# Optimization experiments

Hardware: AMD Instinct MI355X
Metric: run time of the kernel (lower is better)

## Reference

```python
import jax, jax.numpy as jnp
import numpy as np

FLTRSTDEV = 2.0
EXTGRADFAC = 10.0
DMAX = 15.0
ENHANCEMENT = 2.0   # enhancement_factor in the module
NEG_WEIGHT = 1.5    # negative_weight in the module


def make_gauss_edge_fltr(stdev: float) -> np.ndarray:
    """Gaussian-derivative edge filter, shape [2, 1, k, k] (OIHW), k = 2*ceil(2*stdev)+1."""
    r = int(np.ceil(2.0 * stdev))
    x = np.arange(-r, r + 1, dtype=np.float32)
    g = np.exp(-x ** 2 / (2.0 * stdev ** 2)).astype(np.float32)
    g /= g.sum()
    dg = (-x / (stdev ** 2)) * np.exp(-x ** 2 / (2.0 * stdev ** 2))
    dg = (dg / np.abs(dg).sum()).astype(np.float32)
    f_dy = np.outer(dg, g)   # gradient along axis 0
    f_dx = np.outer(g, dg)   # gradient along axis 1
    return np.stack([f_dy, f_dx])[:, None]  # [2,1,k,k]


def cmpt_grad_im(img, fltr):
    """img: [B,1,H,W], fltr: [2,1,k,k] -> [B,2,H,W] gradient image (SAME conv)."""
    return jax.lax.conv_general_dilated(
        img, fltr, window_strides=(1, 1), padding='SAME',
        dimension_numbers=('NCHW', 'OIHW', 'NCHW'))


def setup_inputs() -> dict:
    key = jax.random.key(0)
    k1, k2 = jax.random.split(key)
    B, H, W = 16, 1024, 1024
    # predicted signed distance map, roughly in [-DMAX, DMAX]
    pred_dmap = jax.random.normal(k1, (B, 1, H, W), dtype=jnp.float32) * 5.0
    # stand-in for the snake-rendered signed distance map (detached target)
    snake_dm = jax.random.normal(k2, (B, 1, H, W), dtype=jnp.float32) * 5.0
    fltr = jnp.asarray(make_gauss_edge_fltr(FLTRSTDEV))
    return {"pred_dmap": pred_dmap, "snake_dm": snake_dm, "fltr": fltr}


def reference(pred_dmap, snake_dm, fltr):
    # external-energy gradient images driving the snakes
    gimg = cmpt_grad_im(pred_dmap, fltr) * EXTGRADFAC           # [B,2,H,W]
    gimgW = cmpt_grad_im(jnp.abs(pred_dmap), fltr) * EXTGRADFAC  # [B,2,H,W]
    # dmap[dmap > 0] = dmax  (background set to +dmax)
    sd = jnp.where(snake_dm > 0, DMAX, snake_dm)
    # snake_dm[snake_dm < 0] *= enhancement_factor
    sd = jnp.where(sd < 0, sd * ENHANCEMENT, sd)
    neg_mask = (sd < 0).astype(pred_dmap.dtype)
    squared_diff = (pred_dmap - jax.lax.stop_gradient(sd)) ** 2
    loss = jnp.mean(squared_diff * (1.0 + neg_mask * NEG_WEIGHT))
    return loss, gimg, gimgW
```

## Files before the change

### kernel.cpp

```cpp
#include <hip/hip_runtime.h>

#define HH 1024
#define WW 1024
#define BB 16
#define ROWS 64
#define DMAXC 15.0f
#define ENHC 2.0f
#define NEGWC 1.5f
#define EGFC 10.0f

__device__ __forceinline__ float lossterm(float p, float s) {
    float sd = (s > 0.f) ? DMAXC : s;
    sd = (sd < 0.f) ? sd * ENHC : sd;
    float w = (sd < 0.f) ? (1.f + NEGWC) : 1.f;
    float d = p - sd;
    return d * d * w;
}

__device__ __forceinline__ float rfl(float x) {
    return __uint_as_float(__builtin_amdgcn_readfirstlane(__float_as_uint(x)));
}

#define HROW(SLOT, YIN, DOLOSS)                                               \
    {                                                                         \
        const int yin_ = (YIN);                                               \
        if (lane < 18) {                                                      \
            int gc_ = c0 - 4 + 4 * lane;                                      \
            float4 v_ = make_float4(0.f, 0.f, 0.f, 0.f);                      \
            if ((unsigned)yin_ < HH && (unsigned)gc_ < WW)                    \
                v_ = *(const float4*)&img[(size_t)yin_ * WW + gc_];           \
            *(float4*)&s_row[wid][4 * lane] = v_;                             \
        }                                                                     \
        asm volatile("s_waitcnt lgkmcnt(0)" ::: "memory");                    \
        float wv_[9];                                                         \
        _Pragma("unroll")                                                     \
        for (int k_ = 0; k_ < 9; ++k_) wv_[k_] = s_row[wid][lane + k_];       \
        float hg_ = 0.f, hd_ = 0.f, ag_ = 0.f, ad_ = 0.f;                     \
        _Pragma("unroll")                                                     \
        for (int k_ = 0; k_ < 9; ++k_) {                                      \
            float v_ = wv_[k_];                                               \
            float a_ = fabsf(v_);                                             \
            hg_ += g[k_] * v_;                                                \
            hd_ += dg[k_] * v_;                                               \
            ag_ += g[k_] * a_;                                                \
            ad_ += dg[k_] * a_;                                               \
        }                                                                     \
        hgP[SLOT] = hg_; hdP[SLOT] = hd_;                                     \
        hgA[SLOT] = ag_; hdA[SLOT] = ad_;                                     \
        if (DOLOSS) {                                                         \
            float sv_ = snk[(size_t)yin_ * WW + c0 + lane];                   \
            lsum += lossterm(wv_[4], sv_);                                    \
        }                                                                     \
    }

#define EMIT(YO, BASE)                                                        \
    {                                                                         \
        float c0_ = 0.f, c1_ = 0.f, w0_ = 0.f, w1_ = 0.f;                     \
        _Pragma("unroll")                                                     \
        for (int i_ = 0; i_ < 9; ++i_) {                                      \
            const int s_ = ((BASE) + i_) % 9;            \
            c0_ += dg[i_] * hgP[s_];                                          \
            c1_ += g[i_] * hdP[s_];                                           \
            w0_ += dg[i_] * hgA[s_];                                          \
            w1_ += g[i_] * hdA[s_];                                           \
        }                                                                     \
        size_t o_ = (size_t)(YO) * WW + c0 + lane;                            \
        g0[o_] = EGFC * c0_;                                                  \
        g1[o_] = EGFC * c1_;                                                  \
        g0W[o_] = EGFC * w0_;                                                 \
        g1W[o_] = EGFC * w1_;                                                 \
    }

__global__ __launch_bounds__(256) void snake_rows(
    const float* __restrict__ pred, const float* __restrict__ snake,
    const float* __restrict__ fltr, float* __restrict__ out)
{
    __shared__ float s_row[4][72];
    __shared__ float s_red[4];

    const int t = threadIdx.x;
    const int lane = t & 63;
    const int wid = t >> 6;
    const int b = blockIdx.z;
    const int r0 = blockIdx.y * ROWS;
    const int c0 = blockIdx.x * 256 + wid * 64;

    float g[9], dg[9];
#pragma unroll
    for (int i = 0; i < 9; ++i) {
        float s = 0.f;
#pragma unroll
        for (int j = 0; j < 9; ++j) s += fltr[i * 9 + j];
        dg[i] = rfl(s);
    }
    {
        float inv = 1.f / dg[0];
#pragma unroll
        for (int j = 0; j < 9; ++j) g[j] = rfl(fltr[j] * inv);
    }

    const float* img = pred + (size_t)b * (HH * WW);
    const float* snk = snake + (size_t)b * (HH * WW);
    float* g0 = out + 1 + ((size_t)(b * 2 + 0)) * (HH * WW);
    float* g1 = out + 1 + ((size_t)(b * 2 + 1)) * (HH * WW);
    float* g0W = g0 + (size_t)BB * 2 * HH * WW;
    float* g1W = g1 + (size_t)BB * 2 * HH * WW;

    float hgP[9], hdP[9], hgA[9], hdA[9];
    float lsum = 0.f;

    #pragma unroll
    for (int j = 0; j < 9; ++j) {
        HROW(j, r0 - 4 + j, j >= 4);
    }
    EMIT(r0, 0);

    for (int jj = 9; jj < 72; jj += 9) {
#pragma unroll
        for (int u = 0; u < 9; ++u) {
            const int j = jj + u;
            HROW(u, r0 - 4 + j, j < 68);
            EMIT(r0 + j - 8, (u + 1) % 9);
        }
    }

#pragma unroll
    for (int off = 32; off > 0; off >>= 1) lsum += __shfl_down(lsum, off);
    if (lane == 0) s_red[wid] = lsum;
    __syncthreads();
    if (t == 0) {
        float tot = s_red[0] + s_red[1] + s_red[2] + s_red[3];
        atomicAdd(out, tot * (1.0f / 16777216.0f));
    }
}

extern "C" void kernel_launch(void* const* d_in, const int* in_sizes, int n_in,
                              void* d_out, int out_size, void* d_ws, size_t ws_size,
                              hipStream_t stream) {
    const float* pred = (const float*)d_in[0];
    const float* snake = (const float*)d_in[1];
    const float* fltr = (const float*)d_in[2];
    float* out = (float*)d_out;

    hipMemsetAsync(out, 0, sizeof(float), stream);

    dim3 grid(WW / 256, HH / ROWS, BB);
    snake_rows<<<grid, 256, 0, stream>>>(pred, snake, fltr, out);
}
```

Baseline: 416.8 us.

## Replace LDS row staging with register loads, bpermute halo, and batched prefetch

Drops the per-row shared-memory staging of input rows. Each lane now loads its own element plus an 8-element halo straight into registers and builds the 9-tap window with ds_bpermute. All 9 rows of a group, including the snake values, are loaded before any are consumed, so global loads are batched ahead of compute and each row no longer waits on its own LDS write. Launch bounds also request 4 blocks per SM, which together with the extra prefetch registers risks spills or lower occupancy.

After: 453.4 us. 1.09x slower.

```diff
diff --git a/kernel.cpp b/kernel.cpp
--- a/kernel.cpp
+++ b/kernel.cpp
@@ -21,24 +21,34 @@
     return __uint_as_float(__builtin_amdgcn_readfirstlane(__float_as_uint(x)));
 }
 
-#define HROW(SLOT, YIN, DOLOSS)                                               \
+#define LOADROW(J, LO, HI, SV, DOSNK)                                         \
     {                                                                         \
-        const int yin_ = (YIN);                                               \
-        if (lane < 18) {                                                      \
-            int gc_ = c0 - 4 + 4 * lane;                                      \
-            float4 v_ = make_float4(0.f, 0.f, 0.f, 0.f);                      \
-            if ((unsigned)yin_ < HH && (unsigned)gc_ < WW)                    \
-                v_ = *(const float4*)&img[(size_t)yin_ * WW + gc_];           \
-            *(float4*)&s_row[wid][4 * lane] = v_;                             \
+        const int yin_ = r0 - 4 + (J);                                        \
+        const bool rowok_ = (unsigned)yin_ < HH;                              \
+        const float* rp_ = img + (size_t)yin_ * WW;                           \
+        const int cl_ = c0 - 4 + lane;                                        \
+        LO = (rowok_ && (unsigned)cl_ < WW) ? rp_[cl_] : 0.f;                 \
+        const int ch_ = c0 + 60 + lane;                                       \
+        HI = (rowok_ && lane < 8 && (unsigned)ch_ < WW) ? rp_[ch_] : 0.f;     \
+        SV = (DOSNK) ? snk[(size_t)yin_ * WW + c0 + lane] : 0.f;              \
+    }
+
+#define CONSUME(SLOT, LO, HI, SV, DOLOSS)                                     \
+    {                                                                         \
+        float w_[9];                                                          \
+        w_[0] = LO;                                                           \
+        const int lov_ = __float_as_int(LO);                                  \
+        const int hiv_ = __float_as_int(HI);                                  \
+        _Pragma("unroll")                                                     \
+        for (int k_ = 1; k_ <= 8; ++k_) {                                     \
+            int d_ = __builtin_amdgcn_ds_bpermute(A + 4 * k_, lov_);          \
+            int u_ = __builtin_amdgcn_ds_bpermute(A + 4 * k_, hiv_);          \
+            w_[k_] = __int_as_float((lane + k_ < 64) ? d_ : u_);              \
         }                                                                     \
-        asm volatile("s_waitcnt lgkmcnt(0)" ::: "memory");                    \
-        float wv_[9];                                                         \
-        _Pragma("unroll")                                                     \
-        for (int k_ = 0; k_ < 9; ++k_) wv_[k_] = s_row[wid][lane + k_];       \
         float hg_ = 0.f, hd_ = 0.f, ag_ = 0.f, ad_ = 0.f;                     \
         _Pragma("unroll")                                                     \
         for (int k_ = 0; k_ < 9; ++k_) {                                      \
-            float v_ = wv_[k_];                                               \
+            float v_ = w_[k_];                                                \
             float a_ = fabsf(v_);                                             \
             hg_ += g[k_] * v_;                                                \
             hd_ += dg[k_] * v_;                                               \
@@ -47,10 +57,7 @@
         }                                                                     \
         hgP[SLOT] = hg_; hdP[SLOT] = hd_;                                     \
         hgA[SLOT] = ag_; hdA[SLOT] = ad_;                                     \
-        if (DOLOSS) {                                                         \
-            float sv_ = snk[(size_t)yin_ * WW + c0 + lane];                   \
-            lsum += lossterm(wv_[4], sv_);                                    \
-        }                                                                     \
+        if (DOLOSS) lsum += lossterm(w_[4], SV);                              \
     }
 
 #define EMIT(YO, BASE)                                                        \
@@ -58,24 +65,23 @@
         float c0_ = 0.f, c1_ = 0.f, w0_ = 0.f, w1_ = 0.f;                     \
         _Pragma("unroll")                                                     \
         for (int i_ = 0; i_ < 9; ++i_) {                                      \
-            const int s_ = ((BASE) + i_) % 9;            \
+            const int s_ = ((BASE) + i_) % 9;               \
             c0_ += dg[i_] * hgP[s_];                                          \
             c1_ += g[i_] * hdP[s_];                                           \
             w0_ += dg[i_] * hgA[s_];                                          \
             w1_ += g[i_] * hdA[s_];                                           \
         }                                                                     \
-        size_t o_ = (size_t)(YO) * WW + c0 + lane;                            \
+        const size_t o_ = (size_t)(YO) * WW + c0 + lane;                      \
         g0[o_] = EGFC * c0_;                                                  \
         g1[o_] = EGFC * c1_;                                                  \
         g0W[o_] = EGFC * w0_;                                                 \
         g1W[o_] = EGFC * w1_;                                                 \
     }
 
-__global__ __launch_bounds__(256) void snake_rows(
+__global__ __launch_bounds__(256, 4) void snake_rows(
     const float* __restrict__ pred, const float* __restrict__ snake,
     const float* __restrict__ fltr, float* __restrict__ out)
 {
-    __shared__ float s_row[4][72];
     __shared__ float s_red[4];
 
     const int t = threadIdx.x;
@@ -84,6 +90,7 @@
     const int b = blockIdx.z;
     const int r0 = blockIdx.y * ROWS;
     const int c0 = blockIdx.x * 256 + wid * 64;
+    const int A = lane * 4;
 
     float g[9], dg[9];
 #pragma unroll
@@ -107,19 +114,27 @@
     float* g1W = g1 + (size_t)BB * 2 * HH * WW;
 
     float hgP[9], hdP[9], hgA[9], hdA[9];
+    float loA[9], hiA[9], svA[9];
     float lsum = 0.f;
 
-    #pragma unroll
-    for (int j = 0; j < 9; ++j) {
-        HROW(j, r0 - 4 + j, j >= 4);
-    }
+#pragma unroll
+    for (int u = 0; u < 9; ++u) LOADROW(u, loA[u], hiA[u], svA[u], (u >= 4));
+#pragma unroll
+    for (int u = 0; u < 9; ++u) CONSUME(u, loA[u], hiA[u], svA[u], (u >= 4));
     EMIT(r0, 0);
 
-    for (int jj = 9; jj < 72; jj += 9) {
+#pragma unroll 1
+    for (int m = 0; m < 7; ++m) {
+        const int jbase = 9 + 9 * m;
 #pragma unroll
         for (int u = 0; u < 9; ++u) {
-            const int j = jj + u;
-            HROW(u, r0 - 4 + j, j < 68);
+            const int j = jbase + u;
+            LOADROW(j, loA[u], hiA[u], svA[u], ((unsigned)(j - 4) < 64u));
+        }
+#pragma unroll
+        for (int u = 0; u < 9; ++u) {
+            const int j = jbase + u;
+            CONSUME(u, loA[u], hiA[u], svA[u], ((unsigned)(j - 4) < 64u));
             EMIT(r0 + j - 8, (u + 1) % 9);
         }
     }
```
